# Performance work log

Hardware: AMD Instinct MI355X
Metric: run time of the kernel (lower is better)

Reference implementation:

```python
import jax, jax.numpy as jnp
import numpy as np

IMG = 512.0
B, C, A, H, W, M = 16, 3, 9, 128, 128, 32
K = 5 + C
N = A * H * W


def make_anchors():
    # SSD-style anchor grid: 3 scales x 3 aspect ratios per cell on a HxW grid.
    stride = IMG / H
    cx, cy = jnp.meshgrid(
        (jnp.arange(W, dtype=jnp.float32) + 0.5) * stride,
        (jnp.arange(H, dtype=jnp.float32) + 0.5) * stride,
        indexing='xy')
    scales = jnp.array([16.0, 32.0, 64.0], dtype=jnp.float32)
    ratios = jnp.array([0.5, 1.0, 2.0], dtype=jnp.float32)
    ws = (scales[:, None] * jnp.sqrt(ratios)[None, :]).reshape(-1)  # [A]
    hs = (scales[:, None] / jnp.sqrt(ratios)[None, :]).reshape(-1)
    cx = cx[:, :, None]; cy = cy[:, :, None]  # [H,W,1]
    x1 = cx - ws * 0.5; y1 = cy - hs * 0.5
    x2 = cx + ws * 0.5; y2 = cy + hs * 0.5
    anc = jnp.stack([x1, y1, x2, y2], axis=-1)  # [H,W,A,4]
    return anc.reshape(-1, 4)


def setup_inputs() -> dict:
    key = jax.random.key(0)
    k1, k2, k3, k4 = jax.random.split(key, 4)
    pred = jax.random.normal(k1, (B, A * K, H, W), dtype=jnp.float32)
    anchors = make_anchors()  # [N,4]
    xy = jax.random.uniform(k2, (B, M, 2), minval=0.0, maxval=IMG * 0.8)
    wh = jax.random.uniform(k3, (B, M, 2), minval=16.0, maxval=IMG * 0.2)
    gt_boxes = jnp.concatenate([xy, xy + wh], axis=-1).astype(jnp.float32)
    gt_labels = jax.random.randint(k4, (B, M), 1, C + 1).astype(jnp.int32)
    return {'pred': pred, 'anchors': anchors, 'gt_boxes': gt_boxes, 'gt_labels': gt_labels}


def iou_matrix(anc, boxes):
    # anc [N,4], boxes [M,4] -> [N,M]
    lt = jnp.maximum(anc[:, None, :2], boxes[None, :, :2])
    rb = jnp.minimum(anc[:, None, 2:], boxes[None, :, 2:])
    wh = jnp.clip(rb - lt, 0.0)
    inter = wh[..., 0] * wh[..., 1]
    area_a = (anc[:, 2] - anc[:, 0]) * (anc[:, 3] - anc[:, 1])
    area_b = (boxes[:, 2] - boxes[:, 0]) * (boxes[:, 3] - boxes[:, 1])
    union = area_a[:, None] + area_b[None, :] - inter
    return inter / jnp.maximum(union, 1e-9)


def encode_boxes(anc, boxes):
    ax = (anc[..., 0] + anc[..., 2]) * 0.5
    ay = (anc[..., 1] + anc[..., 3]) * 0.5
    aw = jnp.maximum(anc[..., 2] - anc[..., 0], 1e-6)
    ah = jnp.maximum(anc[..., 3] - anc[..., 1], 1e-6)
    gx = (boxes[..., 0] + boxes[..., 2]) * 0.5
    gy = (boxes[..., 1] + boxes[..., 3]) * 0.5
    gw = jnp.maximum(boxes[..., 2] - boxes[..., 0], 1e-6)
    gh = jnp.maximum(boxes[..., 3] - boxes[..., 1], 1e-6)
    return jnp.stack([(gx - ax) / aw, (gy - ay) / ah,
                      jnp.log(gw / aw), jnp.log(gh / ah)], axis=-1)


def bce_logits(x, t):
    return jnp.maximum(x, 0.0) - x * t + jnp.log1p(jnp.exp(-jnp.abs(x)))


def smooth_l1(d):
    ad = jnp.abs(d)
    return jnp.where(ad < 1.0, 0.5 * d * d, ad - 0.5)


def _detection_loss(pred, anchors, gt_boxes, gt_labels):
    pred = jnp.transpose(pred, (0, 2, 3, 1)).reshape(B, N, K)
    pred_box = pred[..., :4]
    pred_obj = pred[..., 4]
    pred_cls = pred[..., 5:]

    def per_image(pbox, pobj, pcls, gtb, gtl):
        iou = iou_matrix(anchors, gtb)          # [N,M]
        best_iou = jnp.max(iou, axis=1)
        best_idx = jnp.argmax(iou, axis=1)
        pos = best_iou >= 0.5
        neg = best_iou < 0.3
        matched_boxes = gtb[best_idx]           # [N,4]
        matched_labels = gtl[best_idx]          # [N]

        obj_loss = bce_logits(pobj, pos.astype(pobj.dtype))  # [N]

        # hard negative mining on detached loss
        num_pos = jnp.sum(pos)
        num_neg = jnp.sum(neg)
        k = jnp.where(num_pos == 0,
                      jnp.where(num_neg > 0, jnp.maximum(num_neg // 10, 1), 0),
                      jnp.minimum(3 * num_pos, num_neg))
        neg_losses = jnp.where(neg, jax.lax.stop_gradient(obj_loss), -1e9)
        rank = jnp.argsort(jnp.argsort(-neg_losses))  # 0 = largest loss
        sel_neg = neg & (rank < k)
        select = pos | sel_neg
        num_sel = jnp.sum(select)
        obj_sum = jnp.sum(jnp.where(select, obj_loss, 0.0))

        # classification: CE over positives, labels are 1-based
        tgt = jnp.clip(matched_labels - 1, 0, C - 1)
        logp = jax.nn.log_softmax(pcls, axis=-1)
        cls_per = -jnp.take_along_axis(logp, tgt[:, None], axis=1)[:, 0]
        cls_sum = jnp.sum(jnp.where(pos, cls_per, 0.0))

        # localization: smooth L1 over positives
        t = encode_boxes(anchors, matched_boxes)
        loc_per = jnp.sum(smooth_l1(pbox - t), axis=-1)
        loc_sum = jnp.sum(jnp.where(pos, loc_per, 0.0))
        return obj_sum, cls_sum, loc_sum, num_pos, num_sel

    obj_s, cls_s, loc_s, npos, nsel = jax.vmap(per_image)(pred_box, pred_obj, pred_cls, gt_boxes, gt_labels)
    total_pos = jnp.sum(npos)
    total_sel = jnp.sum(nsel)
    denom_pos = jnp.maximum(total_pos, 1).astype(jnp.float32)
    denom_obj = jnp.maximum(total_sel, 1).astype(jnp.float32)
    loss_loc = jnp.sum(loc_s) / denom_pos
    loss_cls = jnp.sum(cls_s) / denom_pos
    loss_obj = jnp.sum(obj_s) / denom_obj
    loss_total = 2.0 * loss_loc + 1.0 * loss_cls + 1.0 * loss_obj
    return jnp.stack([loss_obj, loss_cls, loss_loc, loss_total])


def reference(pred, anchors, gt_boxes, gt_labels):
    return _detection_loss(pred, anchors, gt_boxes, gt_labels)
```

## Files before the change

### kernel.cpp

```cpp
#include <hip/hip_runtime.h>

typedef unsigned long long u64;

#define BB 16
#define CC 3
#define AA 9
#define MM 32
#define KK 8
#define HWSZ 16384
#define NN (AA*HWSZ)

#define STATS_STRIDE 32
#define ST_NPOS 0
#define ST_NNEG 1
#define ST_OBJP 2
#define ST_CLS  3
#define ST_LOC  4
#define ST_K    5
#define ST_TOPK 6

#define KEYS16_WORDS ((size_t)BB*NN/2)
#define STATS_WORDS (BB*STATS_STRIDE)
#define HIST0_WORDS (BB*512)
#define H1_WORDS    (BB*256)
#define CNT_WORDS   4
#define ZERO_WORDS  (STATS_WORDS + HIST0_WORDS + H1_WORDS + CNT_WORDS)

#define HBLK 16
#define SUMMASK ((1ull<<44) - 1ull)
#define ONECNT  (1ull<<44)

__device__ __forceinline__ unsigned calc_k(unsigned np, unsigned nn) {
  if (np == 0u) return (nn > 0u) ? ((nn/10u > 1u) ? nn/10u : 1u) : 0u;
  return (3u*np < nn) ? 3u*np : nn;
}

__device__ __forceinline__ void sel1(unsigned lc, float ls, unsigned r,
                                     unsigned* s_c, float* s_s,
                                     unsigned* s_u, float* s_f,
                                     unsigned& bin_out, unsigned& r_out, float& sab_out)
{
  const int t = threadIdx.x;
  s_c[t] = lc; s_s[t] = ls;
  __syncthreads();
  for (int off = 1; off < 256; off <<= 1) {
    unsigned ac = s_c[t]; float as = s_s[t];
    unsigned bc = 0; float bs = 0.f;
    if (t + off < 256) { bc = s_c[t + off]; bs = s_s[t + off]; }
    __syncthreads();
    s_c[t] = ac + bc; s_s[t] = as + bs;
    __syncthreads();
  }
  bool win = (t == 255) ? (s_c[255] >= r) : (s_c[t] >= r && s_c[t+1] < r);
  if (win) {
    unsigned cum = (t < 255) ? s_c[t+1] : 0u;
    float sab = (t < 255) ? s_s[t+1] : 0.f;
    s_u[0] = (unsigned)t; s_u[1] = r - cum; s_f[0] = sab;
  }
  __syncthreads();
  bin_out = s_u[0]; r_out = s_u[1]; sab_out = s_f[0];
  __syncthreads();
}

__global__ __launch_bounds__(256) void k_zero(uint4* __restrict__ p)
{
  const unsigned i = blockIdx.x * 256u + threadIdx.x;
  if (i < ZERO_WORDS/4) p[i] = make_uint4(0u,0u,0u,0u);
}

__global__ __launch_bounds__(256, 4) void k_main(
    const float* __restrict__ pred,
    const float* __restrict__ gtb, const int* __restrict__ gtl,
    unsigned short* __restrict__ keys16, unsigned* __restrict__ stats,
    u64* __restrict__ hist0)
{
  __shared__ float4 s_box[MM];
  __shared__ float s_area[MM], s_gx[MM], s_gy[MM], s_gw[MM], s_gh[MM];
  __shared__ int s_lab[MM];
  __shared__ int s_list[MM];
  __shared__ int s_cnt;
  __shared__ u64 s_h64[8][257];
  __shared__ unsigned s_ri[2];
  __shared__ float s_rf[3];
  __shared__ unsigned s_plist[AA*256];
  __shared__ unsigned s_pcnt;

  const int tid = threadIdx.x;
  const int b = blockIdx.x >> 6;
  const int t6 = blockIdx.x & 63;
  const int tr = t6 >> 3, tc = t6 & 7;
  const int hrow = tr*16 + (tid >> 4);
  const int wcol = tc*16 + (tid & 15);
  const int hw = hrow*128 + wcol;

  for (int i = tid; i < 8*257; i += 256) (&s_h64[0][0])[i] = 0ull;
  if (tid == 0) { s_ri[0] = 0u; s_ri[1] = 0u; s_pcnt = 0u; }
  if (tid < 3) s_rf[tid] = 0.f;
  if (tid < MM) {
    float x1 = gtb[((size_t)b*MM + tid)*4 + 0];
    float y1 = gtb[((size_t)b*MM + tid)*4 + 1];
    float x2 = gtb[((size_t)b*MM + tid)*4 + 2];
    float y2 = gtb[((size_t)b*MM + tid)*4 + 3];
    s_box[tid] = make_float4(x1, y1, x2, y2);
    s_area[tid] = (x2 - x1) * (y2 - y1);
    s_gx[tid] = (x1 + x2) * 0.5f;
    s_gy[tid] = (y1 + y2) * 0.5f;
    s_gw[tid] = fmaxf(x2 - x1, 1e-6f);
    s_gh[tid] = fmaxf(y2 - y1, 1e-6f);
    s_lab[tid] = gtl[(size_t)b*MM + tid];
  }
  __syncthreads();

  if (tid < 64) {
    const float cxlo = (float)(tc*64 + 2), cxhi = cxlo + 60.f;
    const float cylo = (float)(tr*64 + 2), cyhi = cylo + 60.f;
    bool keep = false;
    if (tid < MM) {
      float4 bx = s_box[tid];
      keep = (bx.z >= cxlo - 46.f) && (bx.x <= cxhi + 46.f) &&
             (bx.w >= cylo - 46.f) && (bx.y <= cyhi + 46.f);
    }
    unsigned long long mask = __ballot(keep);
    if (keep) s_list[__popcll(mask & ((1ull << tid) - 1ull))] = tid;
    if (tid == 0) s_cnt = (int)__popcll(mask);
  }
  __syncthreads();

  const float* pb = pred + (size_t)b * (AA*KK) * HWSZ + hw;
  float xo[AA];
#pragma unroll
  for (int a = 0; a < AA; ++a) xo[a] = pb[(size_t)((a*KK + 4) * HWSZ)];

  const float cx = ((float)wcol + 0.5f) * 4.0f;
  const float cy = ((float)hrow + 0.5f) * 4.0f;
  float AX1[AA], AY1[AA], AX2[AA], AY2[AA], AREA[AA];
  {
    const float S0[3] = {16.f, 32.f, 64.f};
    const float Q0[3] = {0.70710678118654752440f, 1.0f, 1.41421356237309504880f};
#pragma unroll
    for (int i = 0; i < 3; ++i)
#pragma unroll
      for (int jj = 0; jj < 3; ++jj) {
        int a = i*3 + jj;
        float w2 = S0[i] * Q0[jj] * 0.5f;
        float h2 = (S0[i] / Q0[jj]) * 0.5f;
        float x1 = cx - w2, x2 = cx + w2;
        float y1 = cy - h2, y2 = cy + h2;
        AX1[a]=x1; AX2[a]=x2; AY1[a]=y1; AY2[a]=y2;
        AREA[a] = (x2 - x1) * (y2 - y1);
      }
  }

  float bnum[AA], bden[AA]; int bi[AA];
#pragma unroll
  for (int a = 0; a < AA; ++a) { bnum[a] = 0.f; bden[a] = 1.f; bi[a] = 0; }

  const int cnt = s_cnt;
  for (int jj = 0; jj < cnt; ++jj) {
    const int j = s_list[jj];
    const float4 bx = s_box[j];
    const float ba = s_area[j];
#pragma unroll
    for (int a = 0; a < AA; ++a) {
      float lx = fmaxf(AX1[a], bx.x);
      float ly = fmaxf(AY1[a], bx.y);
      float rx = fminf(AX2[a], bx.z);
      float ry = fminf(AY2[a], bx.w);
      float wx = fmaxf(rx - lx, 0.f);
      float wy = fmaxf(ry - ly, 0.f);
      float inter = wx * wy;
      float den = (AREA[a] + ba) - inter;
      bool bt = inter * bden[a] > bnum[a] * den;
      bnum[a] = bt ? inter : bnum[a];
      bden[a] = bt ? den : bden[a];
      bi[a]   = bt ? j : bi[a];
    }
  }

  unsigned short* kout = keys16 + ((size_t)b * AA) * HWSZ + (t6 << 8) + tid;

  const int rep = tid & 7;
  unsigned npos = 0, nneg = 0;
  float objp = 0.f;

#pragma unroll
  for (int a = 0; a < AA; ++a) {
    bool pos = bnum[a] >= 0.5f * bden[a];
    bool neg = bnum[a] < 0.3f * bden[a];

    float x = xo[a];
    float e = __expf(-fabsf(x));
    float ol = fmaxf(x, 0.f) - (pos ? x : 0.f) + __logf(1.f + e);

    unsigned key = 0u;
    if (neg) {
      key = __float_as_uint(ol);
      ++nneg;
      atomicAdd(&s_h64[rep][key >> 24], ONECNT | (u64)(ol * 1048576.0f + 0.5f));
    }
    kout[(size_t)a * HWSZ] = (unsigned short)(key >> 16);

    if (pos) {
      ++npos;
      objp += ol;
      unsigned idx = atomicAdd(&s_pcnt, 1u);
      s_plist[idx] = (unsigned)hw | ((unsigned)a << 14) | ((unsigned)bi[a] << 18);
    }
  }

  __syncthreads();

  float cls2 = 0.f, loc2 = 0.f;
  {
    const int pcnt = (int)s_pcnt;
    const float* pball = pred + (size_t)b * (AA*KK) * HWSZ;
    for (int i = tid; i < pcnt; i += 256) {
      unsigned it = s_plist[i];
      int hw2 = (int)(it & 16383u);
      int a2  = (int)((it >> 14) & 15u);
      int jb  = (int)(it >> 18);
      int w2c = hw2 & 127, h2r = hw2 >> 7;
      float cx2 = ((float)w2c + 0.5f) * 4.0f;
      float cy2 = ((float)h2r + 0.5f) * 4.0f;
      int si = a2 / 3, rj = a2 - si*3;
      float s0 = (si == 0) ? 16.f : ((si == 1) ? 32.f : 64.f);
      float q0 = (rj == 0) ? 0.70710678118654752440f : ((rj == 1) ? 1.0f : 1.41421356237309504880f);
      float w2 = s0 * q0 * 0.5f;
      float h2 = (s0 / q0) * 0.5f;
      float ax1 = cx2 - w2, ax2 = cx2 + w2;
      float ay1 = cy2 - h2, ay2 = cy2 + h2;

      const float* pp = pball + hw2;
      float c0 = pp[(size_t)((a2*KK + 5) * HWSZ)];
      float c1 = pp[(size_t)((a2*KK + 6) * HWSZ)];
      float c2 = pp[(size_t)((a2*KK + 7) * HWSZ)];
      int lab = s_lab[jb];
      int tgt = lab - 1; tgt = tgt < 0 ? 0 : (tgt > CC-1 ? CC-1 : tgt);
      float m = fmaxf(fmaxf(c0, c1), c2);
      float lse = m + __logf(__expf(c0-m) + __expf(c1-m) + __expf(c2-m));
      float ct = (tgt == 0) ? c0 : ((tgt == 1) ? c1 : c2);
      cls2 += lse - ct;

      float axc = (ax1 + ax2) * 0.5f;
      float ayc = (ay1 + ay2) * 0.5f;
      float aw = fmaxf(ax2 - ax1, 1e-6f);
      float ah = fmaxf(ay2 - ay1, 1e-6f);
      float t0 = (s_gx[jb] - axc) / aw;
      float t1 = (s_gy[jb] - ayc) / ah;
      float t2 = __logf(s_gw[jb] / aw);
      float t3 = __logf(s_gh[jb] / ah);
      float p0 = pp[(size_t)((a2*KK + 0) * HWSZ)];
      float p1 = pp[(size_t)((a2*KK + 1) * HWSZ)];
      float p2 = pp[(size_t)((a2*KK + 2) * HWSZ)];
      float p3 = pp[(size_t)((a2*KK + 3) * HWSZ)];
      float l = 0.f, d, ad;
      d = p0-t0; ad = fabsf(d); l += (ad < 1.f) ? 0.5f*d*d : ad - 0.5f;
      d = p1-t1; ad = fabsf(d); l += (ad < 1.f) ? 0.5f*d*d : ad - 0.5f;
      d = p2-t2; ad = fabsf(d); l += (ad < 1.f) ? 0.5f*d*d : ad - 0.5f;
      d = p3-t3; ad = fabsf(d); l += (ad < 1.f) ? 0.5f*d*d : ad - 0.5f;
      loc2 += l;
    }
  }

#pragma unroll
  for (int off = 32; off; off >>= 1) {
    npos += __shfl_down(npos, off);
    nneg += __shfl_down(nneg, off);
    objp += __shfl_down(objp, off);
    cls2 += __shfl_down(cls2, off);
    loc2 += __shfl_down(loc2, off);
  }
  if ((tid & 63) == 0) {
    atomicAdd(&s_ri[0], npos);
    atomicAdd(&s_ri[1], nneg);
    atomicAdd(&s_rf[0], objp);
    atomicAdd(&s_rf[1], cls2);
    atomicAdd(&s_rf[2], loc2);
  }
  __syncthreads();

  unsigned* st = stats + b * STATS_STRIDE;
  if (tid == 0) { atomicAdd(&st[ST_NPOS], s_ri[0]); atomicAdd(&st[ST_NNEG], s_ri[1]); }
  else if (tid == 1) atomicAdd((float*)(st + ST_OBJP), s_rf[0]);
  else if (tid == 2) atomicAdd((float*)(st + ST_CLS), s_rf[1]);
  else if (tid == 3) atomicAdd((float*)(st + ST_LOC), s_rf[2]);

  u64 m = 0ull;
#pragma unroll
  for (int r = 0; r < 8; ++r) m += s_h64[r][tid];
  if (m) atomicAdd(&hist0[b*256 + tid], m);
}

__global__ __launch_bounds__(256) void k_h1(
    const unsigned short* __restrict__ keys16, const unsigned* __restrict__ stats,
    const u64* __restrict__ hist0, unsigned* __restrict__ h1)
{
  __shared__ unsigned s_c[256]; __shared__ float s_s[256];
  __shared__ unsigned s_u[2];   __shared__ float s_f[1];
  __shared__ unsigned s_hc[8][257];
  const int tid = threadIdx.x;
  const int b = blockIdx.x >> 4;
  const unsigned* st = stats + b * STATS_STRIDE;
  const unsigned k = calc_k(st[ST_NPOS], st[ST_NNEG]);
  if (k == 0u) return;

  unsigned bin0, r0; float sab;
  {
    u64 v = hist0[b*256 + tid];
    sel1((unsigned)(v >> 44), (float)(v & SUMMASK) * 0x1p-20f, k,
         s_c, s_s, s_u, s_f, bin0, r0, sab);
  }

  for (int i = tid; i < 8*257; i += 256) (&s_hc[0][0])[i] = 0u;
  __syncthreads();

  const int rep = tid & 7;
  const uint2* kp = (const uint2*)(keys16 + (size_t)b * NN) +
                    (size_t)(blockIdx.x & 15) * 2304;
#pragma unroll
  for (int j = 0; j < 9; ++j) {
    uint2 v = kp[j*256 + tid];
    unsigned k0 = v.x & 0xFFFFu, k1 = v.x >> 16;
    unsigned k2 = v.y & 0xFFFFu, k3 = v.y >> 16;
    if ((k0 >> 8) == bin0) atomicAdd(&s_hc[rep][k0 & 255u], 1u);
    if ((k1 >> 8) == bin0) atomicAdd(&s_hc[rep][k1 & 255u], 1u);
    if ((k2 >> 8) == bin0) atomicAdd(&s_hc[rep][k2 & 255u], 1u);
    if ((k3 >> 8) == bin0) atomicAdd(&s_hc[rep][k3 & 255u], 1u);
  }
  __syncthreads();

  unsigned c = 0;
#pragma unroll
  for (int r = 0; r < 8; ++r) c += s_hc[r][tid];
  if (c) atomicAdd(&h1[b*256 + tid], c);
}

__global__ __launch_bounds__(256) void k_fin(
    const u64* __restrict__ hist0, const unsigned* __restrict__ h1,
    unsigned* __restrict__ stats, unsigned* __restrict__ counter,
    float* __restrict__ out)
{
  __shared__ unsigned s_c[256]; __shared__ float s_s[256];
  __shared__ unsigned s_u[2];   __shared__ float s_f[1];
  __shared__ unsigned s_prev;
  const int b = blockIdx.x;
  const int tid = threadIdx.x;
  unsigned* st = stats + b * STATS_STRIDE;
  const unsigned k = calc_k(st[ST_NPOS], st[ST_NNEG]);
  float topk = 0.f;
  if (k) {
    unsigned bin0, r0, bin1, r1;
    float sab0, sab1;
    {
      u64 v = hist0[b*256 + tid];
      sel1((unsigned)(v >> 44), (float)(v & SUMMASK) * 0x1p-20f, k,
           s_c, s_s, s_u, s_f, bin0, r0, sab0);
    }
    unsigned c1 = h1[b*256 + tid];
    float mid = __uint_as_float((bin0 << 24) | ((unsigned)tid << 16) | 0x8000u);
    sel1(c1, (float)c1 * mid, r0, s_c, s_s, s_u, s_f, bin1, r1, sab1);
    float mid1 = __uint_as_float((bin0 << 24) | (bin1 << 16) | 0x8000u);
    topk = sab0 + sab1 + (float)r1 * mid1;
  }
  if (tid == 0) {
    __hip_atomic_store(&st[ST_K], k, __ATOMIC_RELAXED, __HIP_MEMORY_SCOPE_AGENT);
    __hip_atomic_store((float*)&st[ST_TOPK], topk, __ATOMIC_RELAXED, __HIP_MEMORY_SCOPE_AGENT);
    __threadfence();
    s_prev = __hip_atomic_fetch_add(counter, 1u, __ATOMIC_ACQ_REL, __HIP_MEMORY_SCOPE_AGENT);
  }
  __syncthreads();

  if (s_prev == (unsigned)(BB - 1) && tid < 64) {
    unsigned np = 0, kk = 0;
    float obj = 0.f, cls = 0.f, loc = 0.f;
    if (tid < BB) {
      unsigned* s2 = stats + tid * STATS_STRIDE;
      np  = s2[ST_NPOS];
      cls = ((const float*)s2)[ST_CLS];
      loc = ((const float*)s2)[ST_LOC];
      obj = ((const float*)s2)[ST_OBJP];
      kk  = __hip_atomic_load(&s2[ST_K], __ATOMIC_RELAXED, __HIP_MEMORY_SCOPE_AGENT);
      float tk = __hip_atomic_load((float*)&s2[ST_TOPK], __ATOMIC_ACQUIRE, __HIP_MEMORY_SCOPE_AGENT);
      obj += tk;
    }
#pragma unroll
    for (int off = 8; off; off >>= 1) {
      np  += __shfl_down(np, off);
      kk  += __shfl_down(kk, off);
      obj += __shfl_down(obj, off);
      cls += __shfl_down(cls, off);
      loc += __shfl_down(loc, off);
    }
    if (tid == 0) {
      unsigned ts = np + kk;
      float dp  = (float)(np > 1u ? np : 1u);
      float dob = (float)(ts > 1u ? ts : 1u);
      float lo = obj / dob, lc = cls / dp, ll = loc / dp;
      out[0] = lo;
      out[1] = lc;
      out[2] = ll;
      out[3] = 2.f*ll + lc + lo;
    }
  }
}

extern "C" void kernel_launch(void* const* d_in, const int* in_sizes, int n_in,
                              void* d_out, int out_size, void* d_ws, size_t ws_size,
                              hipStream_t stream)
{
  const float* pred = (const float*)d_in[0];
  const float* gtb  = (const float*)d_in[2];
  const int*   gtl  = (const int*)d_in[3];
  float* out = (float*)d_out;

  unsigned* ws    = (unsigned*)d_ws;
  unsigned short* keys16 = (unsigned short*)ws;
  unsigned* stats = ws + KEYS16_WORDS;
  u64* hist0      = (u64*)(stats + STATS_WORDS);
  unsigned* h1    = (unsigned*)(hist0 + BB*256);
  unsigned* cnt   = h1 + H1_WORDS;

  k_zero<<<(ZERO_WORDS/4 + 255)/256, 256, 0, stream>>>((uint4*)stats);
  k_main<<<BB*64, 256, 0, stream>>>(pred, gtb, gtl, keys16, stats, hist0);
  k_h1<<<BB*HBLK, 256, 0, stream>>>(keys16, stats, hist0, h1);
  k_fin<<<BB, 256, 0, stream>>>(hist0, h1, stats, cnt, out);
}
```

Before: 37.96 us.

## Replace global atomics with per-block partials and drop the zeroing kernel

Each k_main block now writes its histogram and stats to its own slot instead of doing global atomicAdds, and k_h1/k_fin reduce the 64 per-block partials themselves. This lets the separate k_zero launch go away, saving one kernel launch and atomic contention on the shared histogram. The counter is now reset inside k_h1. In exchange, each k_h1 and k_fin block re-reads 64x256 u64 partials, which adds memory traffic and redundant reductions across the 16 k_h1 blocks per image.

```diff
diff --git a/kernel.cpp b/kernel.cpp
--- a/kernel.cpp
+++ b/kernel.cpp
@@ -10,25 +10,18 @@
 #define HWSZ 16384
 #define NN (AA*HWSZ)
 
-#define STATS_STRIDE 32
-#define ST_NPOS 0
-#define ST_NNEG 1
-#define ST_OBJP 2
-#define ST_CLS  3
-#define ST_LOC  4
-#define ST_K    5
-#define ST_TOPK 6
-
 #define KEYS16_WORDS ((size_t)BB*NN/2)
-#define STATS_WORDS (BB*STATS_STRIDE)
-#define HIST0_WORDS (BB*512)
-#define H1_WORDS    (BB*256)
-#define CNT_WORDS   4
-#define ZERO_WORDS  (STATS_WORDS + HIST0_WORDS + H1_WORDS + CNT_WORDS)
-
+#define NBLK (BB*64)
 #define HBLK 16
 #define SUMMASK ((1ull<<44) - 1ull)
 #define ONECNT  (1ull<<44)
+
+#define S2_NP 0
+#define S2_K  1
+#define S2_OBJ 2
+#define S2_CLS 3
+#define S2_LOC 4
+#define S2_TOPK 5
 
 __device__ __forceinline__ unsigned calc_k(unsigned np, unsigned nn) {
   if (np == 0u) return (nn > 0u) ? ((nn/10u > 1u) ? nn/10u : 1u) : 0u;
@@ -62,17 +55,11 @@
   __syncthreads();
 }
 
-__global__ __launch_bounds__(256) void k_zero(uint4* __restrict__ p)
-{
-  const unsigned i = blockIdx.x * 256u + threadIdx.x;
-  if (i < ZERO_WORDS/4) p[i] = make_uint4(0u,0u,0u,0u);
-}
-
 __global__ __launch_bounds__(256, 4) void k_main(
     const float* __restrict__ pred,
     const float* __restrict__ gtb, const int* __restrict__ gtl,
-    unsigned short* __restrict__ keys16, unsigned* __restrict__ stats,
-    u64* __restrict__ hist0)
+    unsigned short* __restrict__ keys16, unsigned* __restrict__ stats_pb,
+    u64* __restrict__ hist_pb)
 {
   __shared__ float4 s_box[MM];
   __shared__ float s_area[MM], s_gx[MM], s_gy[MM], s_gw[MM], s_gh[MM];
@@ -279,37 +266,53 @@
   }
   __syncthreads();
 
-  unsigned* st = stats + b * STATS_STRIDE;
-  if (tid == 0) { atomicAdd(&st[ST_NPOS], s_ri[0]); atomicAdd(&st[ST_NNEG], s_ri[1]); }
-  else if (tid == 1) atomicAdd((float*)(st + ST_OBJP), s_rf[0]);
-  else if (tid == 2) atomicAdd((float*)(st + ST_CLS), s_rf[1]);
-  else if (tid == 3) atomicAdd((float*)(st + ST_LOC), s_rf[2]);
+  unsigned* srow = stats_pb + (size_t)blockIdx.x * 8;
+  if (tid == 0) { srow[0] = s_ri[0]; srow[1] = s_ri[1]; }
+  else if (tid == 1) ((float*)srow)[2] = s_rf[0];
+  else if (tid == 2) ((float*)srow)[3] = s_rf[1];
+  else if (tid == 3) ((float*)srow)[4] = s_rf[2];
 
   u64 m = 0ull;
 #pragma unroll
   for (int r = 0; r < 8; ++r) m += s_h64[r][tid];
-  if (m) atomicAdd(&hist0[b*256 + tid], m);
+  hist_pb[(size_t)blockIdx.x * 256 + tid] = m;
 }
 
 __global__ __launch_bounds__(256) void k_h1(
-    const unsigned short* __restrict__ keys16, const unsigned* __restrict__ stats,
-    const u64* __restrict__ hist0, unsigned* __restrict__ h1)
+    const unsigned short* __restrict__ keys16, const unsigned* __restrict__ stats_pb,
+    const u64* __restrict__ hist_pb, unsigned* __restrict__ h1_pb,
+    unsigned* __restrict__ cnt)
 {
   __shared__ unsigned s_c[256]; __shared__ float s_s[256];
   __shared__ unsigned s_u[2];   __shared__ float s_f[1];
   __shared__ unsigned s_hc[8][257];
+  __shared__ unsigned s_np, s_nn;
   const int tid = threadIdx.x;
   const int b = blockIdx.x >> 4;
-  const unsigned* st = stats + b * STATS_STRIDE;
-  const unsigned k = calc_k(st[ST_NPOS], st[ST_NNEG]);
-  if (k == 0u) return;
-
+
+  if (tid == 0) cnt[0] = 0u;
+
+  if (tid < 64) {
+    unsigned np = stats_pb[(size_t)(b*64 + tid)*8 + 0];
+    unsigned nn = stats_pb[(size_t)(b*64 + tid)*8 + 1];
+#pragma unroll
+    for (int off = 32; off; off >>= 1) { np += __shfl_down(np, off); nn += __shfl_down(nn, off); }
+    if (tid == 0) { s_np = np; s_nn = nn; }
+  }
+  __syncthreads();
+  const unsigned k = calc_k(s_np, s_nn);
+  unsigned* hout = h1_pb + (size_t)(blockIdx.x) * 256;
+  if (k == 0u) { hout[tid] = 0u; return; }
+
+  u64 hv = 0ull;
+  {
+    const u64* hp = hist_pb + (size_t)b * 64 * 256 + tid;
+#pragma unroll 8
+    for (int i = 0; i < 64; ++i) hv += hp[(size_t)i * 256];
+  }
   unsigned bin0, r0; float sab;
-  {
-    u64 v = hist0[b*256 + tid];
-    sel1((unsigned)(v >> 44), (float)(v & SUMMASK) * 0x1p-20f, k,
-         s_c, s_s, s_u, s_f, bin0, r0, sab);
-  }
+  sel1((unsigned)(hv >> 44), (float)(hv & SUMMASK) * 0x1p-20f, k,
+       s_c, s_s, s_u, s_f, bin0, r0, sab);
 
   for (int i = tid; i < 8*257; i += 256) (&s_hc[0][0])[i] = 0u;
   __syncthreads();
@@ -332,56 +335,85 @@
   unsigned c = 0;
 #pragma unroll
   for (int r = 0; r < 8; ++r) c += s_hc[r][tid];
-  if (c) atomicAdd(&h1[b*256 + tid], c);
+  hout[tid] = c;
 }
 
 __global__ __launch_bounds__(256) void k_fin(
-    const u64* __restrict__ hist0, const unsigned* __restrict__ h1,
-    unsigned* __restrict__ stats, unsigned* __restrict__ counter,
-    float* __restrict__ out)
+    const unsigned* __restrict__ stats_pb, const u64* __restrict__ hist_pb,
+    const unsigned* __restrict__ h1_pb, unsigned* __restrict__ stats2,
+    unsigned* __restrict__ counter, float* __restrict__ out)
 {
   __shared__ unsigned s_c[256]; __shared__ float s_s[256];
   __shared__ unsigned s_u[2];   __shared__ float s_f[1];
+  __shared__ unsigned s_np, s_nn;
+  __shared__ float s_obj, s_cls, s_loc;
   __shared__ unsigned s_prev;
   const int b = blockIdx.x;
   const int tid = threadIdx.x;
-  unsigned* st = stats + b * STATS_STRIDE;
-  const unsigned k = calc_k(st[ST_NPOS], st[ST_NNEG]);
+
+  if (tid < 64) {
+    const unsigned* sp = stats_pb + (size_t)(b*64 + tid)*8;
+    unsigned np = sp[0], nn = sp[1];
+    float ob = ((const float*)sp)[2];
+    float cl = ((const float*)sp)[3];
+    float lo = ((const float*)sp)[4];
+#pragma unroll
+    for (int off = 32; off; off >>= 1) {
+      np += __shfl_down(np, off); nn += __shfl_down(nn, off);
+      ob += __shfl_down(ob, off); cl += __shfl_down(cl, off); lo += __shfl_down(lo, off);
+    }
+    if (tid == 0) { s_np = np; s_nn = nn; s_obj = ob; s_cls = cl; s_loc = lo; }
+  }
+  __syncthreads();
+  const unsigned k = calc_k(s_np, s_nn);
   float topk = 0.f;
   if (k) {
+    u64 hv = 0ull;
+    {
+      const u64* hp = hist_pb + (size_t)b * 64 * 256 + tid;
+#pragma unroll 8
+      for (int i = 0; i < 64; ++i) hv += hp[(size_t)i * 256];
+    }
     unsigned bin0, r0, bin1, r1;
     float sab0, sab1;
+    sel1((unsigned)(hv >> 44), (float)(hv & SUMMASK) * 0x1p-20f, k,
+         s_c, s_s, s_u, s_f, bin0, r0, sab0);
+    unsigned c1 = 0;
     {
-      u64 v = hist0[b*256 + tid];
-      sel1((unsigned)(v >> 44), (float)(v & SUMMASK) * 0x1p-20f, k,
-           s_c, s_s, s_u, s_f, bin0, r0, sab0);
-    }
-    unsigned c1 = h1[b*256 + tid];
+      const unsigned* hp1 = h1_pb + (size_t)b * 16 * 256 + tid;
+#pragma unroll
+      for (int i = 0; i < 16; ++i) c1 += hp1[i * 256];
+    }
     float mid = __uint_as_float((bin0 << 24) | ((unsigned)tid << 16) | 0x8000u);
     sel1(c1, (float)c1 * mid, r0, s_c, s_s, s_u, s_f, bin1, r1, sab1);
     float mid1 = __uint_as_float((bin0 << 24) | (bin1 << 16) | 0x8000u);
     topk = sab0 + sab1 + (float)r1 * mid1;
   }
   if (tid == 0) {
-    __hip_atomic_store(&st[ST_K], k, __ATOMIC_RELAXED, __HIP_MEMORY_SCOPE_AGENT);
-    __hip_atomic_store((float*)&st[ST_TOPK], topk, __ATOMIC_RELAXED, __HIP_MEMORY_SCOPE_AGENT);
+    unsigned* s2 = stats2 + b * 8;
+    __hip_atomic_store(&s2[S2_NP], s_np, __ATOMIC_RELAXED, __HIP_MEMORY_SCOPE_AGENT);
+    __hip_atomic_store(&s2[S2_K],  k,    __ATOMIC_RELAXED, __HIP_MEMORY_SCOPE_AGENT);
+    __hip_atomic_store((float*)&s2[S2_OBJ], s_obj, __ATOMIC_RELAXED, __HIP_MEMORY_SCOPE_AGENT);
+    __hip_atomic_store((float*)&s2[S2_CLS], s_cls, __ATOMIC_RELAXED, __HIP_MEMORY_SCOPE_AGENT);
+    __hip_atomic_store((float*)&s2[S2_LOC], s_loc, __ATOMIC_RELAXED, __HIP_MEMORY_SCOPE_AGENT);
+    __hip_atomic_store((float*)&s2[S2_TOPK], topk, __ATOMIC_RELAXED, __HIP_MEMORY_SCOPE_AGENT);
     __threadfence();
     s_prev = __hip_atomic_fetch_add(counter, 1u, __ATOMIC_ACQ_REL, __HIP_MEMORY_SCOPE_AGENT);
   }
   __syncthreads();
 
   if (s_prev == (unsigned)(BB - 1) && tid < 64) {
+    __threadfence();
     unsigned np = 0, kk = 0;
     float obj = 0.f, cls = 0.f, loc = 0.f;
     if (tid < BB) {
-      unsigned* s2 = stats + tid * STATS_STRIDE;
-      np  = s2[ST_NPOS];
-      cls = ((const float*)s2)[ST_CLS];
-      loc = ((const float*)s2)[ST_LOC];
-      obj = ((const float*)s2)[ST_OBJP];
-      kk  = __hip_atomic_load(&s2[ST_K], __ATOMIC_RELAXED, __HIP_MEMORY_SCOPE_AGENT);
-      float tk = __hip_atomic_load((float*)&s2[ST_TOPK], __ATOMIC_ACQUIRE, __HIP_MEMORY_SCOPE_AGENT);
-      obj += tk;
+      unsigned* s2 = stats2 + tid * 8;
+      np  = __hip_atomic_load(&s2[S2_NP], __ATOMIC_RELAXED, __HIP_MEMORY_SCOPE_AGENT);
+      kk  = __hip_atomic_load(&s2[S2_K],  __ATOMIC_RELAXED, __HIP_MEMORY_SCOPE_AGENT);
+      obj = __hip_atomic_load((float*)&s2[S2_OBJ], __ATOMIC_RELAXED, __HIP_MEMORY_SCOPE_AGENT)
+          + __hip_atomic_load((float*)&s2[S2_TOPK], __ATOMIC_ACQUIRE, __HIP_MEMORY_SCOPE_AGENT);
+      cls = __hip_atomic_load((float*)&s2[S2_CLS], __ATOMIC_RELAXED, __HIP_MEMORY_SCOPE_AGENT);
+      loc = __hip_atomic_load((float*)&s2[S2_LOC], __ATOMIC_RELAXED, __HIP_MEMORY_SCOPE_AGENT);
     }
 #pragma unroll
     for (int off = 8; off; off >>= 1) {
@@ -415,13 +447,13 @@
 
   unsigned* ws    = (unsigned*)d_ws;
   unsigned short* keys16 = (unsigned short*)ws;
-  unsigned* stats = ws + KEYS16_WORDS;
-  u64* hist0      = (u64*)(stats + STATS_WORDS);
-  unsigned* h1    = (unsigned*)(hist0 + BB*256);
-  unsigned* cnt   = h1 + H1_WORDS;
-
-  k_zero<<<(ZERO_WORDS/4 + 255)/256, 256, 0, stream>>>((uint4*)stats);
-  k_main<<<BB*64, 256, 0, stream>>>(pred, gtb, gtl, keys16, stats, hist0);
-  k_h1<<<BB*HBLK, 256, 0, stream>>>(keys16, stats, hist0, h1);
-  k_fin<<<BB, 256, 0, stream>>>(hist0, h1, stats, cnt, out);
-}
+  u64* hist_pb    = (u64*)(ws + KEYS16_WORDS);
+  unsigned* stats_pb = (unsigned*)(hist_pb + (size_t)NBLK*256);
+  unsigned* h1_pb = stats_pb + NBLK*8;
+  unsigned* stats2 = h1_pb + 256*256;
+  unsigned* cnt   = stats2 + BB*8;
+
+  k_main<<<NBLK, 256, 0, stream>>>(pred, gtb, gtl, keys16, stats_pb, hist_pb);
+  k_h1<<<BB*HBLK, 256, 0, stream>>>(keys16, stats_pb, hist_pb, h1_pb, cnt);
+  k_fin<<<BB, 256, 0, stream>>>(stats_pb, hist_pb, h1_pb, stats2, cnt, out);
+}
```

New measurement: 40.03 us. +5.4%, slower.
